# Performance work log

Measured on AMD Instinct MI355X. Metric: run time of the kernel, lower is better.

## Reference

```python
import jax, jax.numpy as jnp
import numpy as np

N, E, IN, H, C, EDIM, G, NC = 20000, 200000, 512, 4, 64, 384, 64, 751
NEG_GATV2 = 0.2   # leaky_relu slope inside GATv2 attention
NEG_ACT = 0.01    # F.leaky_relu default between layers


def _w(key, shape):
    return jax.random.normal(key, shape, dtype=jnp.float32) * 0.05


def setup_inputs() -> dict:
    key = jax.random.key(0)
    ks = jax.random.split(key, 24)
    x = jax.random.normal(ks[0], (N, IN), dtype=jnp.float32)
    edge_index = jax.random.randint(ks[1], (2, E), 0, N, dtype=jnp.int32)
    edge_attr = jax.random.normal(ks[2], (E, EDIM), dtype=jnp.float32)
    batch = (jnp.arange(N, dtype=jnp.int32) * G) // N  # sorted, covers all G graphs
    return {
        "x": x, "edge_index": edge_index, "edge_attr": edge_attr, "batch": batch,
        # GATv2 layer 1 (512 -> 4 heads x 64, concat)
        "W1l": _w(ks[3], (IN, H * C)), "b1l": jnp.zeros((H * C,), jnp.float32),
        "W1r": _w(ks[4], (IN, H * C)), "b1r": jnp.zeros((H * C,), jnp.float32),
        "W1e": _w(ks[5], (EDIM, H * C)),
        "att1": _w(ks[6], (H, C)), "bias1": jnp.zeros((H * C,), jnp.float32),
        # GATv2 layer 2 (256 -> 1 head x 64)
        "W2l": _w(ks[7], (H * C, C)), "b2l": jnp.zeros((C,), jnp.float32),
        "W2r": _w(ks[8], (H * C, C)), "b2r": jnp.zeros((C,), jnp.float32),
        "W2e": _w(ks[9], (EDIM, C)),
        "att2": _w(ks[10], (1, C)), "bias2": jnp.zeros((C,), jnp.float32),
        # LayerNorm + classifier
        "ln_g": jnp.ones((C,), jnp.float32), "ln_b": jnp.zeros((C,), jnp.float32),
        "clf_W": _w(ks[11], (C, NC)), "clf_b": jnp.zeros((NC,), jnp.float32),
    }


def gatv2_layer(x, ei_i, ei_j, ea, Wl, bl, Wr, br, We, att, bias, heads, outc):
    n = x.shape[0]
    xl = (x @ Wl + bl).reshape(n, heads, outc)  # source-side transform (x_j)
    xr = (x @ Wr + br).reshape(n, heads, outc)  # target-side transform (x_i)
    ep = (ea @ We).reshape(-1, heads, outc)     # lin_edge has no bias in PyG
    m = jax.nn.leaky_relu(xl[ei_j] + xr[ei_i] + ep, NEG_GATV2)  # [E',H,C]
    logit = jnp.einsum('ehc,hc->eh', m, att)
    lmax = jax.ops.segment_max(logit, ei_i, num_segments=n)
    ex = jnp.exp(logit - lmax[ei_i])
    den = jax.ops.segment_sum(ex, ei_i, num_segments=n)
    alpha = ex / den[ei_i]                                       # segment softmax
    out = jax.ops.segment_sum(xl[ei_j] * alpha[:, :, None], ei_i, num_segments=n)
    return out.reshape(n, heads * outc) + bias, alpha


def reference(x, edge_index, edge_attr, batch, W1l, b1l, W1r, b1r, W1e, att1, bias1,
              W2l, b2l, W2r, b2r, W2e, att2, bias2, ln_g, ln_b, clf_W, clf_b):
    n = x.shape[0]
    row, col = edge_index[0], edge_index[1]
    # add_self_loops with fill_value='mean': loop attr = scatter-mean over edge_index[1]
    cnt = jax.ops.segment_sum(jnp.ones_like(edge_attr[:, 0]), col, num_segments=n)
    loop_attr = jax.ops.segment_sum(edge_attr, col, num_segments=n) / jnp.maximum(cnt, 1.0)[:, None]
    loops = jnp.arange(n, dtype=row.dtype)
    # flow='target_to_source': aggregate at i=edge_index[0], messages from j=edge_index[1]
    ei_i = jnp.concatenate([row, loops])
    ei_j = jnp.concatenate([col, loops])
    ea = jnp.concatenate([edge_attr, loop_attr], axis=0)

    h1, _ = gatv2_layer(x, ei_i, ei_j, ea, W1l, b1l, W1r, b1r, W1e, att1, bias1, H, C)
    h1 = jax.nn.leaky_relu(h1, NEG_ACT)
    h2, _ = gatv2_layer(h1, ei_i, ei_j, ea, W2l, b2l, W2r, b2r, W2e, att2, bias2, 1, C)
    h2 = jax.nn.leaky_relu(h2, NEG_ACT)

    g = jax.ops.segment_max(h2, batch, num_segments=G)  # global_max_pool -> [G, C]
    mu = g.mean(axis=-1, keepdims=True)
    var = g.var(axis=-1, keepdims=True)
    gn = (g - mu) / jnp.sqrt(var + 1e-5) * ln_g + ln_b
    cls_score = gn @ clf_W + clf_b
    return cls_score, gn
```

## Files before the change

### kernel.cpp

```cpp
#include <hip/hip_runtime.h>

#define NN 20000
#define NE 200000
#define NH1 256
#define ED 384
#define NG 64
#define NCLS 751
#define ETOT (NE + NN)

typedef unsigned short u16;
typedef __attribute__((ext_vector_type(8))) short short8;
typedef __attribute__((ext_vector_type(4))) float f32x4;

__device__ __forceinline__ float bf2f(u16 u){
  union { unsigned int i; float f; } v; v.i = ((unsigned int)u) << 16; return v.f;
}
__device__ __forceinline__ u16 f2bf(float f){
  union { float f; unsigned int i; } v; v.f = f;
  return (u16)((v.i + 0x7fffu + ((v.i >> 16) & 1u)) >> 16);
}

__global__ void transpose_k(const float* __restrict__ in, u16* __restrict__ out, int K, int N){
  int idx = blockIdx.x * 256 + threadIdx.x;
  if (idx >= K * N) return;
  int k = idx / N, n = idx - k * N;
  out[n * K + k] = f2bf(in[idx]);
}

__global__ void convx_k(const float* __restrict__ in, u16* __restrict__ out, int total8){
  int idx = blockIdx.x * 256 + threadIdx.x;
  if (idx >= total8) return;
  const float4* p = (const float4*)in + (size_t)idx * 2;
  float4 f0 = p[0], f1 = p[1];
  union { u16 h[8]; uint4 v; } pk;
  pk.h[0] = f2bf(f0.x); pk.h[1] = f2bf(f0.y); pk.h[2] = f2bf(f0.z); pk.h[3] = f2bf(f0.w);
  pk.h[4] = f2bf(f1.x); pk.h[5] = f2bf(f1.y); pk.h[6] = f2bf(f1.z); pk.h[7] = f2bf(f1.w);
  ((uint4*)out)[idx] = pk.v;
}

__global__ void concatbias_k(const float* __restrict__ b1l, const float* __restrict__ b1r,
                             const float* __restrict__ b2l, const float* __restrict__ b2r,
                             float* __restrict__ biasLR1, float* __restrict__ biasLR2){
  int i = blockIdx.x * 256 + threadIdx.x;
  if (i < 256) biasLR1[i] = b1l[i];
  else if (i < 512) biasLR1[i] = b1r[i - 256];
  else if (i < 576) biasLR2[i - 512] = b2l[i - 512];
  else if (i < 640) biasLR2[i - 512] = b2r[i - 576];
}

__global__ void hist_k(const int* __restrict__ rowA, const int* __restrict__ colA,
                       int* __restrict__ degR, int* __restrict__ degC){
  int e = blockIdx.x * 256 + threadIdx.x;
  if (e >= NE) return;
  atomicAdd(&degR[rowA[e]], 1);
  atomicAdd(&degC[colA[e]], 1);
}

__global__ void scan_k(const int* __restrict__ degR, const int* __restrict__ degC,
                       int* __restrict__ rowPtr, int* __restrict__ colPtr){
  __shared__ int sR[256], sC[256];
  int t = threadIdx.x;
  const int chunk = (NN + 255) / 256;
  int beg = t * chunk, end = min(beg + chunk, NN);
  int aR = 0, aC = 0;
  for (int i = beg; i < end; i++){ aR += degR[i]; aC += degC[i]; }
  sR[t] = aR; sC[t] = aC;
  __syncthreads();
  for (int off = 1; off < 256; off <<= 1){
    int vR = 0, vC = 0;
    if (t >= off){ vR = sR[t - off]; vC = sC[t - off]; }
    __syncthreads();
    sR[t] += vR; sC[t] += vC;
    __syncthreads();
  }
  int rR = (t == 0) ? 0 : sR[t - 1];
  int rC = (t == 0) ? 0 : sC[t - 1];
  for (int i = beg; i < end; i++){
    rowPtr[i] = rR; rR += degR[i];
    colPtr[i] = rC; rC += degC[i];
  }
  if (t == 255){ rowPtr[NN] = sR[255]; colPtr[NN] = sC[255]; }
}

__global__ void scatter_k(const int* __restrict__ rowA, const int* __restrict__ colA,
                          const int* __restrict__ rowPtr, const int* __restrict__ colPtr,
                          int* __restrict__ rowCur, int* __restrict__ colCur,
                          int* __restrict__ rowIdx, int* __restrict__ colIdx){
  int e = blockIdx.x * 256 + threadIdx.x;
  if (e >= NE) return;
  int r = rowA[e]; int p = atomicAdd(&rowCur[r], 1); rowIdx[rowPtr[r] + p] = e;
  int c = colA[e]; int q = atomicAdd(&colCur[c], 1); colIdx[colPtr[c] + q] = e;
}

__global__ __launch_bounds__(256) void loopattr_k(const int* __restrict__ colPtr,
                                                  const int* __restrict__ colIdx,
                                                  const float* __restrict__ eattr,
                                                  u16* __restrict__ ea16){
  int node = blockIdx.x * 4 + (threadIdx.x >> 6);
  if (node >= NN) return;
  int lane = threadIdx.x & 63;
  int p0 = colPtr[node], deg = colPtr[node + 1] - p0;
  float inv = 1.f / fmaxf((float)deg, 1.f);
  float s[6] = {0.f, 0.f, 0.f, 0.f, 0.f, 0.f};
  for (int t = 0; t < deg; t++){
    int e = colIdx[p0 + t];
    const float* rowp = eattr + (size_t)e * ED;
    u16* wp = ea16 + (size_t)e * ED;
    #pragma unroll
    for (int c0 = 0; c0 < 6; c0++){
      float v = rowp[c0 * 64 + lane];
      s[c0] += v;
      wp[c0 * 64 + lane] = f2bf(v);
    }
  }
  u16* outp = ea16 + (size_t)(NE + node) * ED;
  #pragma unroll
  for (int c0 = 0; c0 < 6; c0++) outp[c0 * 64 + lane] = f2bf(s[c0] * inv);
}

__global__ __launch_bounds__(256)
void gemm_k(const u16* __restrict__ A16,
            const u16* __restrict__ Bt, int M, int K, int Ntot,
            const float* __restrict__ bias, u16* __restrict__ outBf)
{
  __shared__ __align__(16) u16 lA[128 * 40];
  __shared__ __align__(16) u16 lB[64 * 40];
  const int tid  = threadIdx.x;
  const int lane = tid & 63;
  const int wave = tid >> 6;
  const int m0 = blockIdx.x * 128;
  const int n0 = blockIdx.y * 64;
  const int lr  = tid >> 2;
  const int lkc = (tid & 3) << 3;
  const int lm = lane & 15;
  const int lk = (lane >> 4) << 3;
  const int wrow = wave << 5;

  f32x4 acc[2][4];
  #pragma unroll
  for (int i = 0; i < 2; i++)
    #pragma unroll
    for (int j = 0; j < 4; j++) acc[i][j] = (f32x4){0.f, 0.f, 0.f, 0.f};

  const u16* aB0 = A16 + (size_t)(m0 + lr) * K + lkc;
  const u16* aB1 = A16 + (size_t)(m0 + lr + 64) * K + lkc;
  const u16* bB  = Bt + (size_t)(n0 + lr) * K + lkc;

  uint4 rA0, rA1, rB;

#define GEMM_ISSUE(K0) \
  { rA0 = *(const uint4*)(aB0 + (K0)); \
    rA1 = *(const uint4*)(aB1 + (K0)); \
    rB  = *(const uint4*)(bB  + (K0)); }

  GEMM_ISSUE(0);
  for (int k0 = 0; k0 < K; k0 += 32){
    *(uint4*)(&lA[lr * 40 + lkc]) = rA0;
    *(uint4*)(&lA[(lr + 64) * 40 + lkc]) = rA1;
    *(uint4*)(&lB[lr * 40 + lkc]) = rB;
    __syncthreads();
    if (k0 + 32 < K) GEMM_ISSUE(k0 + 32);
    short8 a0 = *(const short8*)(&lA[(wrow + lm) * 40 + lk]);
    short8 a1 = *(const short8*)(&lA[(wrow + 16 + lm) * 40 + lk]);
    #pragma unroll
    for (int nj = 0; nj < 4; nj++){
      short8 b = *(const short8*)(&lB[(nj * 16 + lm) * 40 + lk]);
      acc[0][nj] = __builtin_amdgcn_mfma_f32_16x16x32_bf16(a0, b, acc[0][nj], 0, 0, 0);
      acc[1][nj] = __builtin_amdgcn_mfma_f32_16x16x32_bf16(a1, b, acc[1][nj], 0, 0, 0);
    }
    __syncthreads();
  }
#undef GEMM_ISSUE

  #pragma unroll
  for (int mi = 0; mi < 2; mi++)
    #pragma unroll
    for (int r4 = 0; r4 < 4; r4++){
      int row = wrow + mi * 16 + ((lane >> 4) << 2) + r4;
      int gm = m0 + row;
      if (gm < M){
        #pragma unroll
        for (int nj = 0; nj < 4; nj++){
          int gc = n0 + nj * 16 + lm;
          outBf[(size_t)gm * Ntot + gc] = f2bf(acc[mi][nj][r4] + bias[gc]);
        }
      }
    }
}

__global__ __launch_bounds__(256)
void edge_k(const u16* __restrict__ ea16,
            const u16* __restrict__ BtE,
            const int* __restrict__ rowA, const int* __restrict__ colA,
            const u16* __restrict__ XLR1,
            const float* __restrict__ att1,
            float* __restrict__ logit1,
            u16* __restrict__ ep2)
{
  __shared__ __align__(16) u16 lA[64 * 40];
  __shared__ __align__(16) u16 lB[320 * 40];
  const int tid = threadIdx.x;
  const int lane = tid & 63;
  const int wave = tid >> 6;
  const int m0 = blockIdx.x * 64;
  const int lm = lane & 15;
  const int lk = (lane >> 4) << 3;
  const int arow = tid >> 2;
  const int akc = (tid & 3) << 3;

  f32x4 acc[4][5];
  #pragma unroll
  for (int i = 0; i < 4; i++)
    #pragma unroll
    for (int j = 0; j < 5; j++) acc[i][j] = (f32x4){0.f, 0.f, 0.f, 0.f};

  const int gmA = m0 + arow;
  const u16* aBase = ea16 + (size_t)gmA * ED + akc;
  const u16* bBase = BtE + (size_t)arow * ED + akc;

  uint4 pA, pB0, pB1, pB2, pB3, pB4;

#define EDGE_ISSUE(K0) \
  { pA  = *(const uint4*)(aBase + (K0)); \
    const u16* bp = bBase + (K0); \
    pB0 = *(const uint4*)(bp); \
    pB1 = *(const uint4*)(bp + (size_t)64 * ED); \
    pB2 = *(const uint4*)(bp + (size_t)128 * ED); \
    pB3 = *(const uint4*)(bp + (size_t)192 * ED); \
    pB4 = *(const uint4*)(bp + (size_t)256 * ED); }

  EDGE_ISSUE(0);
  for (int k0 = 0; k0 < ED; k0 += 32){
    *(uint4*)(&lA[arow * 40 + akc]) = pA;
    *(uint4*)(&lB[(arow      ) * 40 + akc]) = pB0;
    *(uint4*)(&lB[(arow +  64) * 40 + akc]) = pB1;
    *(uint4*)(&lB[(arow + 128) * 40 + akc]) = pB2;
    *(uint4*)(&lB[(arow + 192) * 40 + akc]) = pB3;
    *(uint4*)(&lB[(arow + 256) * 40 + akc]) = pB4;
    __syncthreads();
    if (k0 + 32 < ED) EDGE_ISSUE(k0 + 32);
    short8 a[4];
    #pragma unroll
    for (int mi = 0; mi < 4; mi++) a[mi] = *(const short8*)(&lA[(mi * 16 + lm) * 40 + lk]);
    #pragma unroll
    for (int nj = 0; nj < 4; nj++){
      short8 b = *(const short8*)(&lB[(wave * 64 + nj * 16 + lm) * 40 + lk]);
      #pragma unroll
      for (int mi = 0; mi < 4; mi++)
        acc[mi][nj] = __builtin_amdgcn_mfma_f32_16x16x32_bf16(a[mi], b, acc[mi][nj], 0, 0, 0);
    }
    {
      short8 b = *(const short8*)(&lB[(256 + wave * 16 + lm) * 40 + lk]);
      #pragma unroll
      for (int mi = 0; mi < 4; mi++)
        acc[mi][4] = __builtin_amdgcn_mfma_f32_16x16x32_bf16(a[mi], b, acc[mi][4], 0, 0, 0);
    }
    __syncthreads();
  }
#undef EDGE_ISSUE

  float attc[4];
  #pragma unroll
  for (int nj = 0; nj < 4; nj++) attc[nj] = att1[wave * 64 + nj * 16 + lm];
  const int quad4 = (lane >> 4) << 2;
  #pragma unroll
  for (int mi = 0; mi < 4; mi++)
    #pragma unroll
    for (int r4 = 0; r4 < 4; r4++){
      int e = m0 + mi * 16 + quad4 + r4;
      float partial = 0.f;
      if (e < ETOT){
        int ii = (e < NE) ? rowA[e] : (e - NE);
        int jj = (e < NE) ? colA[e] : (e - NE);
        const u16* xlp = XLR1 + (size_t)jj * 512 + wave * 64;
        const u16* xrp = XLR1 + (size_t)ii * 512 + 256 + wave * 64;
        #pragma unroll
        for (int nj = 0; nj < 4; nj++){
          float v = acc[mi][nj][r4] + bf2f(xlp[nj * 16 + lm]) + bf2f(xrp[nj * 16 + lm]);
          v = (v > 0.f) ? v : 0.2f * v;
          partial += v * attc[nj];
        }
        ep2[(size_t)e * 64 + wave * 16 + lm] = f2bf(acc[mi][4][r4]);
      }
      partial += __shfl_xor(partial, 1);
      partial += __shfl_xor(partial, 2);
      partial += __shfl_xor(partial, 4);
      partial += __shfl_xor(partial, 8);
      if (lm == 0 && e < ETOT) logit1[(size_t)e * 4 + wave] = partial;
    }
}

__global__ __launch_bounds__(256) void logit2_k(const int* __restrict__ rowA,
    const int* __restrict__ colA, const u16* __restrict__ ep2,
    const u16* __restrict__ XLR2,
    const float* __restrict__ att2, float* __restrict__ logit2)
{
  int e = blockIdx.x * 16 + (threadIdx.x >> 4);
  if (e >= ETOT) return;
  int lm = threadIdx.x & 15;
  int ii = (e < NE) ? rowA[e] : (e - NE);
  int jj = (e < NE) ? colA[e] : (e - NE);
  ushort4 pe = *(const ushort4*)(ep2 + (size_t)e * 64 + lm * 4);
  ushort4 pl = *(const ushort4*)(XLR2 + (size_t)jj * 128 + lm * 4);
  ushort4 pr = *(const ushort4*)(XLR2 + (size_t)ii * 128 + 64 + lm * 4);
  float s = 0.f;
  float v0 = bf2f(pe.x) + bf2f(pl.x) + bf2f(pr.x); v0 = v0 > 0.f ? v0 : 0.2f * v0;
  float v1 = bf2f(pe.y) + bf2f(pl.y) + bf2f(pr.y); v1 = v1 > 0.f ? v1 : 0.2f * v1;
  float v2 = bf2f(pe.z) + bf2f(pl.z) + bf2f(pr.z); v2 = v2 > 0.f ? v2 : 0.2f * v2;
  float v3 = bf2f(pe.w) + bf2f(pl.w) + bf2f(pr.w); v3 = v3 > 0.f ? v3 : 0.2f * v3;
  s = v0 * att2[lm * 4] + v1 * att2[lm * 4 + 1] + v2 * att2[lm * 4 + 2] + v3 * att2[lm * 4 + 3];
  s += __shfl_xor(s, 1);
  s += __shfl_xor(s, 2);
  s += __shfl_xor(s, 4);
  s += __shfl_xor(s, 8);
  if (lm == 0) logit2[e] = s;
}

__global__ __launch_bounds__(256) void agg1_k(const int* __restrict__ rowPtr,
    const int* __restrict__ rowIdx, const float4* __restrict__ lg4,
    const u16* __restrict__ XL1, int xstride, const int* __restrict__ colA,
    const float* __restrict__ bias1, u16* __restrict__ H1)
{
  int node = blockIdx.x * 4 + (threadIdx.x >> 6);
  if (node >= NN) return;
  int lane = threadIdx.x & 63;
  int p0 = rowPtr[node], deg = rowPtr[node + 1] - p0;
  float4 sl = lg4[NE + node];
  float m0 = sl.x, m1 = sl.y, m2 = sl.z, m3 = sl.w;
  for (int t = lane; t < deg; t += 64){
    float4 l = lg4[rowIdx[p0 + t]];
    m0 = fmaxf(m0, l.x); m1 = fmaxf(m1, l.y); m2 = fmaxf(m2, l.z); m3 = fmaxf(m3, l.w);
  }
  #pragma unroll
  for (int off = 32; off > 0; off >>= 1){
    m0 = fmaxf(m0, __shfl_xor(m0, off));
    m1 = fmaxf(m1, __shfl_xor(m1, off));
    m2 = fmaxf(m2, __shfl_xor(m2, off));
    m3 = fmaxf(m3, __shfl_xor(m3, off));
  }
  float d0, d1, d2, d3, a0, a1, a2, a3;
  {
    float e0 = __expf(sl.x - m0), e1 = __expf(sl.y - m1), e2 = __expf(sl.z - m2), e3 = __expf(sl.w - m3);
    d0 = e0; d1 = e1; d2 = e2; d3 = e3;
    const u16* xp = XL1 + (size_t)node * xstride;
    a0 = e0 * bf2f(xp[lane]); a1 = e1 * bf2f(xp[64 + lane]);
    a2 = e2 * bf2f(xp[128 + lane]); a3 = e3 * bf2f(xp[192 + lane]);
  }
  int t = 0;
  for (; t + 1 < deg; t += 2){
    int eA = rowIdx[p0 + t];
    int eB = rowIdx[p0 + t + 1];
    float4 lA_ = lg4[eA];
    float4 lB_ = lg4[eB];
    int jA = colA[eA];
    int jB = colA[eB];
    const u16* xa = XL1 + (size_t)jA * xstride;
    const u16* xb = XL1 + (size_t)jB * xstride;
    float eA0 = __expf(lA_.x - m0), eA1 = __expf(lA_.y - m1), eA2 = __expf(lA_.z - m2), eA3 = __expf(lA_.w - m3);
    float eB0 = __expf(lB_.x - m0), eB1 = __expf(lB_.y - m1), eB2 = __expf(lB_.z - m2), eB3 = __expf(lB_.w - m3);
    d0 += eA0 + eB0; d1 += eA1 + eB1; d2 += eA2 + eB2; d3 += eA3 + eB3;
    a0 += eA0 * bf2f(xa[lane])       + eB0 * bf2f(xb[lane]);
    a1 += eA1 * bf2f(xa[64 + lane])  + eB1 * bf2f(xb[64 + lane]);
    a2 += eA2 * bf2f(xa[128 + lane]) + eB2 * bf2f(xb[128 + lane]);
    a3 += eA3 * bf2f(xa[192 + lane]) + eB3 * bf2f(xb[192 + lane]);
  }
  if (t < deg){
    int e = rowIdx[p0 + t];
    float4 l = lg4[e];
    int j = colA[e];
    float e0 = __expf(l.x - m0), e1 = __expf(l.y - m1), e2 = __expf(l.z - m2), e3 = __expf(l.w - m3);
    d0 += e0; d1 += e1; d2 += e2; d3 += e3;
    const u16* xp = XL1 + (size_t)j * xstride;
    a0 += e0 * bf2f(xp[lane]); a1 += e1 * bf2f(xp[64 + lane]);
    a2 += e2 * bf2f(xp[128 + lane]); a3 += e3 * bf2f(xp[192 + lane]);
  }
  float v0 = a0 / d0 + bias1[lane];
  float v1 = a1 / d1 + bias1[64 + lane];
  float v2 = a2 / d2 + bias1[128 + lane];
  float v3 = a3 / d3 + bias1[192 + lane];
  v0 = v0 > 0.f ? v0 : 0.01f * v0;
  v1 = v1 > 0.f ? v1 : 0.01f * v1;
  v2 = v2 > 0.f ? v2 : 0.01f * v2;
  v3 = v3 > 0.f ? v3 : 0.01f * v3;
  u16* hp = H1 + (size_t)node * NH1;
  hp[lane] = f2bf(v0); hp[64 + lane] = f2bf(v1);
  hp[128 + lane] = f2bf(v2); hp[192 + lane] = f2bf(v3);
}

__global__ __launch_bounds__(256) void agg2_k(const int* __restrict__ rowPtr,
    const int* __restrict__ rowIdx, const float* __restrict__ lg,
    const u16* __restrict__ XL2, int xstride, const int* __restrict__ colA,
    const float* __restrict__ bias2, float* __restrict__ H2)
{
  int node = blockIdx.x * 4 + (threadIdx.x >> 6);
  if (node >= NN) return;
  int lane = threadIdx.x & 63;
  int p0 = rowPtr[node], deg = rowPtr[node + 1] - p0;
  float sl = lg[NE + node];
  float mx = sl;
  for (int t = lane; t < deg; t += 64) mx = fmaxf(mx, lg[rowIdx[p0 + t]]);
  #pragma unroll
  for (int off = 32; off > 0; off >>= 1) mx = fmaxf(mx, __shfl_xor(mx, off));
  float den = __expf(sl - mx);
  float acc = den * bf2f(XL2[(size_t)node * xstride + lane]);
  int t = 0;
  for (; t + 1 < deg; t += 2){
    int eA = rowIdx[p0 + t];
    int eB = rowIdx[p0 + t + 1];
    float exA = __expf(lg[eA] - mx);
    float exB = __expf(lg[eB] - mx);
    int jA = colA[eA];
    int jB = colA[eB];
    den += exA + exB;
    acc += exA * bf2f(XL2[(size_t)jA * xstride + lane])
         + exB * bf2f(XL2[(size_t)jB * xstride + lane]);
  }
  if (t < deg){
    int e = rowIdx[p0 + t];
    float ex = __expf(lg[e] - mx);
    den += ex;
    acc += ex * bf2f(XL2[(size_t)colA[e] * xstride + lane]);
  }
  float v = acc / den + bias2[lane];
  v = v > 0.f ? v : 0.01f * v;
  H2[(size_t)node * 64 + lane] = v;
}

__global__ __launch_bounds__(256) void poolln_k(const float* __restrict__ H2,
    const float* __restrict__ lng, const float* __restrict__ lnb, float* __restrict__ outGn)
{
  __shared__ float sm[4][64];
  int g = blockIdx.x, w = threadIdx.x >> 6, c = threadIdx.x & 63;
  int beg = (g * NN + NG - 1) / NG;
  int end = ((g + 1) * NN + NG - 1) / NG;
  float m = -3.0e38f;
  for (int n = beg + w; n < end; n += 4) m = fmaxf(m, H2[(size_t)n * 64 + c]);
  sm[w][c] = m;
  __syncthreads();
  if (threadIdx.x < 64){
    m = fmaxf(fmaxf(sm[0][c], sm[1][c]), fmaxf(sm[2][c], sm[3][c]));
    float s = m;
    #pragma unroll
    for (int off = 32; off > 0; off >>= 1) s += __shfl_xor(s, off);
    float mu = s * (1.f / 64.f);
    float d = m - mu;
    float vv = d * d;
    #pragma unroll
    for (int off = 32; off > 0; off >>= 1) vv += __shfl_xor(vv, off);
    float var = vv * (1.f / 64.f);
    outGn[g * 64 + c] = d * rsqrtf(var + 1e-5f) * lng[c] + lnb[c];
  }
}

__global__ __launch_bounds__(256) void clf_k(const float* __restrict__ gn,
    const float* __restrict__ W, const float* __restrict__ b, float* __restrict__ outCls)
{
  __shared__ float sg[64];
  int g = blockIdx.x;
  if (threadIdx.x < 64) sg[threadIdx.x] = gn[g * 64 + threadIdx.x];
  __syncthreads();
  for (int o = threadIdx.x; o < NCLS; o += 256){
    float s = b[o];
    #pragma unroll 16
    for (int c = 0; c < 64; c++) s += sg[c] * W[c * NCLS + o];
    outCls[(size_t)g * NCLS + o] = s;
  }
}

extern "C" void kernel_launch(void* const* d_in, const int* in_sizes, int n_in,
                              void* d_out, int out_size, void* d_ws, size_t ws_size,
                              hipStream_t stream)
{
  const float* x     = (const float*)d_in[0];
  const int*   eidx  = (const int*)d_in[1];
  const float* eattr = (const float*)d_in[2];
  const float* W1l = (const float*)d_in[4];
  const float* b1l = (const float*)d_in[5];
  const float* W1r = (const float*)d_in[6];
  const float* b1r = (const float*)d_in[7];
  const float* W1e = (const float*)d_in[8];
  const float* att1 = (const float*)d_in[9];
  const float* bias1 = (const float*)d_in[10];
  const float* W2l = (const float*)d_in[11];
  const float* b2l = (const float*)d_in[12];
  const float* W2r = (const float*)d_in[13];
  const float* b2r = (const float*)d_in[14];
  const float* W2e = (const float*)d_in[15];
  const float* att2 = (const float*)d_in[16];
  const float* bias2 = (const float*)d_in[17];
  const float* lng = (const float*)d_in[18];
  const float* lnb = (const float*)d_in[19];
  const float* clfW = (const float*)d_in[20];
  const float* clfb = (const float*)d_in[21];
  const int* rowA = eidx;
  const int* colA = eidx + NE;

  char* w = (char*)d_ws;
  auto alloc = [&](size_t b) -> char* {
    char* p = w; w += (b + 255) & ~(size_t)255; return p;
  };
  u16* W1lrT  = (u16*)alloc((size_t)512 * 512 * 2);
  u16* BtE    = (u16*)alloc((size_t)320 * ED * 2);
  u16* W2lrT  = (u16*)alloc((size_t)128 * 256 * 2);
  float* biasLR1 = (float*)alloc(512 * 4);
  float* biasLR2 = (float*)alloc(128 * 4);
  int* degR   = (int*)alloc((size_t)NN * 4);
  int* degC   = (int*)alloc((size_t)NN * 4);
  int* rowPtr = (int*)alloc((size_t)(NN + 1) * 4);
  int* colPtr = (int*)alloc((size_t)(NN + 1) * 4);
  int* rowCur = (int*)alloc((size_t)NN * 4);
  int* colCur = (int*)alloc((size_t)NN * 4);
  int* rowIdx = (int*)alloc((size_t)NE * 4);
  int* colIdx = (int*)alloc((size_t)NE * 4);
  u16* ea16   = (u16*)alloc((size_t)ETOT * ED * 2);
  u16* x16    = (u16*)alloc((size_t)NN * 512 * 2);
  u16* XLR1   = (u16*)alloc((size_t)NN * 512 * 2);
  float* logit1 = (float*)alloc((size_t)ETOT * 4 * 4);
  u16* H1     = (u16*)alloc((size_t)NN * NH1 * 2);
  u16* ep2    = (u16*)alloc((size_t)ETOT * 64 * 2);
  u16* XLR2   = (u16*)ea16;
  float* logit2 = (float*)((char*)ea16 + (size_t)5500928);
  float* H2   = (float*)((char*)ea16 + (size_t)6553600);

  hipMemsetAsync(degR, 0, (size_t)NN * 4, stream);
  hipMemsetAsync(degC, 0, (size_t)NN * 4, stream);
  hipMemsetAsync(rowCur, 0, (size_t)NN * 4, stream);
  hipMemsetAsync(colCur, 0, (size_t)NN * 4, stream);

  transpose_k<<<(512 * 256 + 255) / 256, 256, 0, stream>>>(W1l, W1lrT, 512, 256);
  transpose_k<<<(512 * 256 + 255) / 256, 256, 0, stream>>>(W1r, W1lrT + (size_t)256 * 512, 512, 256);
  transpose_k<<<(ED * 256 + 255) / 256, 256, 0, stream>>>(W1e, BtE, ED, 256);
  transpose_k<<<(ED * 64 + 255) / 256, 256, 0, stream>>>(W2e, BtE + (size_t)256 * ED, ED, 64);
  transpose_k<<<(256 * 64 + 255) / 256, 256, 0, stream>>>(W2l, W2lrT, 256, 64);
  transpose_k<<<(256 * 64 + 255) / 256, 256, 0, stream>>>(W2r, W2lrT + (size_t)64 * 256, 256, 64);
  concatbias_k<<<3, 256, 0, stream>>>(b1l, b1r, b2l, b2r, biasLR1, biasLR2);
  convx_k<<<(NN * 512 / 8 + 255) / 256, 256, 0, stream>>>(x, x16, NN * 512 / 8);

  hist_k<<<(NE + 255) / 256, 256, 0, stream>>>(rowA, colA, degR, degC);
  scan_k<<<1, 256, 0, stream>>>(degR, degC, rowPtr, colPtr);
  scatter_k<<<(NE + 255) / 256, 256, 0, stream>>>(rowA, colA, rowPtr, colPtr,
                                                  rowCur, colCur, rowIdx, colIdx);
  loopattr_k<<<(NN + 3) / 4, 256, 0, stream>>>(colPtr, colIdx, eattr, ea16);

  dim3 gx1((NN + 127) / 128, 8);
  gemm_k<<<gx1, 256, 0, stream>>>(x16, W1lrT, NN, 512, 512, biasLR1, XLR1);
  edge_k<<<(ETOT + 63) / 64, 256, 0, stream>>>(ea16, BtE, rowA, colA,
                                               XLR1, att1, logit1, ep2);
  agg1_k<<<(NN + 3) / 4, 256, 0, stream>>>(rowPtr, rowIdx, (const float4*)logit1,
                                           XLR1, 512, colA, bias1, H1);
  dim3 gx2((NN + 127) / 128, 2);
  gemm_k<<<gx2, 256, 0, stream>>>(H1, W2lrT, NN, 256, 128, biasLR2, XLR2);
  logit2_k<<<(ETOT + 15) / 16, 256, 0, stream>>>(rowA, colA, ep2, XLR2, att2, logit2);
  agg2_k<<<(NN + 3) / 4, 256, 0, stream>>>(rowPtr, rowIdx, logit2, XLR2, 128, colA, bias2, H2);

  float* outCls = (float*)d_out;
  float* outGn  = outCls + (size_t)NG * NCLS;
  poolln_k<<<NG, 256, 0, stream>>>(H2, lng, lnb, outGn);
  clf_k<<<NG, 256, 0, stream>>>(outGn, clfW, clfb, outCls);
}
```

Measured before the change: 962.7 us.

## Widen GEMM N-tile to 128 and deepen A prefetch in GEMM and edge kernels

The node GEMM now computes 128x128 tiles per block instead of 128x64, halving grid columns and reusing each A tile across twice as many MFMAs. Both the node GEMM and the edge GEMM unroll the K loop by two and prefetch A fragments two steps ahead to hide global latency. The edge kernel also gets an occupancy hint of four blocks per CU. Trade-offs are higher register pressure from doubled accumulators, fewer blocks for the smaller second GEMM, and prefetches that read slightly past the last K slice.

```diff
diff --git a/kernel.cpp b/kernel.cpp
--- a/kernel.cpp
+++ b/kernel.cpp
@@ -124,53 +124,74 @@
             const float* __restrict__ bias, u16* __restrict__ outBf)
 {
   __shared__ __align__(16) u16 lA[128 * 40];
-  __shared__ __align__(16) u16 lB[64 * 40];
+  __shared__ __align__(16) u16 lB[128 * 40];
   const int tid  = threadIdx.x;
   const int lane = tid & 63;
   const int wave = tid >> 6;
   const int m0 = blockIdx.x * 128;
-  const int n0 = blockIdx.y * 64;
+  const int n0 = blockIdx.y * 128;
   const int lr  = tid >> 2;
   const int lkc = (tid & 3) << 3;
   const int lm = lane & 15;
   const int lk = (lane >> 4) << 3;
   const int wrow = wave << 5;
 
-  f32x4 acc[2][4];
+  f32x4 acc[2][8];
   #pragma unroll
   for (int i = 0; i < 2; i++)
     #pragma unroll
-    for (int j = 0; j < 4; j++) acc[i][j] = (f32x4){0.f, 0.f, 0.f, 0.f};
+    for (int j = 0; j < 8; j++) acc[i][j] = (f32x4){0.f, 0.f, 0.f, 0.f};
 
   const u16* aB0 = A16 + (size_t)(m0 + lr) * K + lkc;
   const u16* aB1 = A16 + (size_t)(m0 + lr + 64) * K + lkc;
-  const u16* bB  = Bt + (size_t)(n0 + lr) * K + lkc;
-
-  uint4 rA0, rA1, rB;
-
-#define GEMM_ISSUE(K0) \
-  { rA0 = *(const uint4*)(aB0 + (K0)); \
-    rA1 = *(const uint4*)(aB1 + (K0)); \
-    rB  = *(const uint4*)(bB  + (K0)); }
-
-  GEMM_ISSUE(0);
-  for (int k0 = 0; k0 < K; k0 += 32){
-    *(uint4*)(&lA[lr * 40 + lkc]) = rA0;
-    *(uint4*)(&lA[(lr + 64) * 40 + lkc]) = rA1;
-    *(uint4*)(&lB[lr * 40 + lkc]) = rB;
-    __syncthreads();
-    if (k0 + 32 < K) GEMM_ISSUE(k0 + 32);
-    short8 a0 = *(const short8*)(&lA[(wrow + lm) * 40 + lk]);
-    short8 a1 = *(const short8*)(&lA[(wrow + 16 + lm) * 40 + lk]);
-    #pragma unroll
-    for (int nj = 0; nj < 4; nj++){
-      short8 b = *(const short8*)(&lB[(nj * 16 + lm) * 40 + lk]);
-      acc[0][nj] = __builtin_amdgcn_mfma_f32_16x16x32_bf16(a0, b, acc[0][nj], 0, 0, 0);
-      acc[1][nj] = __builtin_amdgcn_mfma_f32_16x16x32_bf16(a1, b, acc[1][nj], 0, 0, 0);
-    }
-    __syncthreads();
-  }
-#undef GEMM_ISSUE
+  const u16* bB0 = Bt + (size_t)(n0 + lr) * K + lkc;
+  const u16* bB1 = Bt + (size_t)(n0 + lr + 64) * K + lkc;
+
+  uint4 rAa0, rAa1, rAb0, rAb1, rB0, rB1;
+
+#define GSTORE(RA0, RA1) \
+  { *(uint4*)(&lA[lr * 40 + lkc]) = RA0; \
+    *(uint4*)(&lA[(lr + 64) * 40 + lkc]) = RA1; \
+    *(uint4*)(&lB[lr * 40 + lkc]) = rB0; \
+    *(uint4*)(&lB[(lr + 64) * 40 + lkc]) = rB1; }
+
+#define GCOMP \
+  { short8 a0 = *(const short8*)(&lA[(wrow + lm) * 40 + lk]); \
+    short8 a1 = *(const short8*)(&lA[(wrow + 16 + lm) * 40 + lk]); \
+    _Pragma("unroll") \
+    for (int nj = 0; nj < 8; nj++){ \
+      short8 b = *(const short8*)(&lB[(nj * 16 + lm) * 40 + lk]); \
+      acc[0][nj] = __builtin_amdgcn_mfma_f32_16x16x32_bf16(a0, b, acc[0][nj], 0, 0, 0); \
+      acc[1][nj] = __builtin_amdgcn_mfma_f32_16x16x32_bf16(a1, b, acc[1][nj], 0, 0, 0); \
+    } }
+
+  rAa0 = *(const uint4*)(aB0);
+  rAa1 = *(const uint4*)(aB1);
+  rAb0 = *(const uint4*)(aB0 + 32);
+  rAb1 = *(const uint4*)(aB1 + 32);
+  rB0  = *(const uint4*)(bB0);
+  rB1  = *(const uint4*)(bB1);
+
+  for (int k0 = 0; k0 < K; k0 += 64){
+    GSTORE(rAa0, rAa1);
+    __syncthreads();
+    rAa0 = *(const uint4*)(aB0 + k0 + 64);
+    rAa1 = *(const uint4*)(aB1 + k0 + 64);
+    rB0  = *(const uint4*)(bB0 + k0 + 32);
+    rB1  = *(const uint4*)(bB1 + k0 + 32);
+    GCOMP;
+    __syncthreads();
+    GSTORE(rAb0, rAb1);
+    __syncthreads();
+    rAb0 = *(const uint4*)(aB0 + k0 + 96);
+    rAb1 = *(const uint4*)(aB1 + k0 + 96);
+    rB0  = *(const uint4*)(bB0 + k0 + 64);
+    rB1  = *(const uint4*)(bB1 + k0 + 64);
+    GCOMP;
+    __syncthreads();
+  }
+#undef GSTORE
+#undef GCOMP
 
   #pragma unroll
   for (int mi = 0; mi < 2; mi++)
@@ -180,7 +201,7 @@
       int gm = m0 + row;
       if (gm < M){
         #pragma unroll
-        for (int nj = 0; nj < 4; nj++){
+        for (int nj = 0; nj < 8; nj++){
           int gc = n0 + nj * 16 + lm;
           outBf[(size_t)gm * Ntot + gc] = f2bf(acc[mi][nj][r4] + bias[gc]);
         }
@@ -188,7 +209,7 @@
     }
 }
 
-__global__ __launch_bounds__(256)
+__global__ __launch_bounds__(256, 4)
 void edge_k(const u16* __restrict__ ea16,
             const u16* __restrict__ BtE,
             const int* __restrict__ rowA, const int* __restrict__ colA,
@@ -218,46 +239,61 @@
   const u16* aBase = ea16 + (size_t)gmA * ED + akc;
   const u16* bBase = BtE + (size_t)arow * ED + akc;
 
-  uint4 pA, pB0, pB1, pB2, pB3, pB4;
-
-#define EDGE_ISSUE(K0) \
-  { pA  = *(const uint4*)(aBase + (K0)); \
-    const u16* bp = bBase + (K0); \
+  uint4 pAa, pAb, pB0, pB1, pB2, pB3, pB4;
+
+#define EISS_B(K0) \
+  { const u16* bp = bBase + (K0); \
     pB0 = *(const uint4*)(bp); \
     pB1 = *(const uint4*)(bp + (size_t)64 * ED); \
     pB2 = *(const uint4*)(bp + (size_t)128 * ED); \
     pB3 = *(const uint4*)(bp + (size_t)192 * ED); \
     pB4 = *(const uint4*)(bp + (size_t)256 * ED); }
 
-  EDGE_ISSUE(0);
-  for (int k0 = 0; k0 < ED; k0 += 32){
-    *(uint4*)(&lA[arow * 40 + akc]) = pA;
-    *(uint4*)(&lB[(arow      ) * 40 + akc]) = pB0;
-    *(uint4*)(&lB[(arow +  64) * 40 + akc]) = pB1;
-    *(uint4*)(&lB[(arow + 128) * 40 + akc]) = pB2;
-    *(uint4*)(&lB[(arow + 192) * 40 + akc]) = pB3;
-    *(uint4*)(&lB[(arow + 256) * 40 + akc]) = pB4;
-    __syncthreads();
-    if (k0 + 32 < ED) EDGE_ISSUE(k0 + 32);
-    short8 a[4];
-    #pragma unroll
-    for (int mi = 0; mi < 4; mi++) a[mi] = *(const short8*)(&lA[(mi * 16 + lm) * 40 + lk]);
-    #pragma unroll
-    for (int nj = 0; nj < 4; nj++){
-      short8 b = *(const short8*)(&lB[(wave * 64 + nj * 16 + lm) * 40 + lk]);
-      #pragma unroll
-      for (int mi = 0; mi < 4; mi++)
-        acc[mi][nj] = __builtin_amdgcn_mfma_f32_16x16x32_bf16(a[mi], b, acc[mi][nj], 0, 0, 0);
-    }
-    {
-      short8 b = *(const short8*)(&lB[(256 + wave * 16 + lm) * 40 + lk]);
-      #pragma unroll
-      for (int mi = 0; mi < 4; mi++)
-        acc[mi][4] = __builtin_amdgcn_mfma_f32_16x16x32_bf16(a[mi], b, acc[mi][4], 0, 0, 0);
-    }
-    __syncthreads();
-  }
-#undef EDGE_ISSUE
+#define ESTORE(PA) \
+  { *(uint4*)(&lA[arow * 40 + akc]) = PA; \
+    *(uint4*)(&lB[(arow      ) * 40 + akc]) = pB0; \
+    *(uint4*)(&lB[(arow +  64) * 40 + akc]) = pB1; \
+    *(uint4*)(&lB[(arow + 128) * 40 + akc]) = pB2; \
+    *(uint4*)(&lB[(arow + 192) * 40 + akc]) = pB3; \
+    *(uint4*)(&lB[(arow + 256) * 40 + akc]) = pB4; }
+
+#define ECOMP \
+  { short8 a[4]; \
+    _Pragma("unroll") \
+    for (int mi = 0; mi < 4; mi++) a[mi] = *(const short8*)(&lA[(mi * 16 + lm) * 40 + lk]); \
+    _Pragma("unroll") \
+    for (int nj = 0; nj < 4; nj++){ \
+      short8 b = *(const short8*)(&lB[(wave * 64 + nj * 16 + lm) * 40 + lk]); \
+      _Pragma("unroll") \
+      for (int mi = 0; mi < 4; mi++) \
+        acc[mi][nj] = __builtin_amdgcn_mfma_f32_16x16x32_bf16(a[mi], b, acc[mi][nj], 0, 0, 0); \
+    } \
+    { short8 b = *(const short8*)(&lB[(256 + wave * 16 + lm) * 40 + lk]); \
+      _Pragma("unroll") \
+      for (int mi = 0; mi < 4; mi++) \
+        acc[mi][4] = __builtin_amdgcn_mfma_f32_16x16x32_bf16(a[mi], b, acc[mi][4], 0, 0, 0); } }
+
+  pAa = *(const uint4*)(aBase);
+  pAb = *(const uint4*)(aBase + 32);
+  EISS_B(0);
+
+  for (int k0 = 0; k0 < ED; k0 += 64){
+    ESTORE(pAa);
+    __syncthreads();
+    pAa = *(const uint4*)(aBase + k0 + 64);
+    EISS_B(k0 + 32);
+    ECOMP;
+    __syncthreads();
+    ESTORE(pAb);
+    __syncthreads();
+    pAb = *(const uint4*)(aBase + k0 + 96);
+    EISS_B(k0 + 64);
+    ECOMP;
+    __syncthreads();
+  }
+#undef EISS_B
+#undef ESTORE
+#undef ECOMP
 
   float attc[4];
   #pragma unroll
@@ -542,13 +578,13 @@
                                                   rowCur, colCur, rowIdx, colIdx);
   loopattr_k<<<(NN + 3) / 4, 256, 0, stream>>>(colPtr, colIdx, eattr, ea16);
 
-  dim3 gx1((NN + 127) / 128, 8);
+  dim3 gx1((NN + 127) / 128, 4);
   gemm_k<<<gx1, 256, 0, stream>>>(x16, W1lrT, NN, 512, 512, biasLR1, XLR1);
   edge_k<<<(ETOT + 63) / 64, 256, 0, stream>>>(ea16, BtE, rowA, colA,
                                                XLR1, att1, logit1, ep2);
   agg1_k<<<(NN + 3) / 4, 256, 0, stream>>>(rowPtr, rowIdx, (const float4*)logit1,
                                            XLR1, 512, colA, bias1, H1);
-  dim3 gx2((NN + 127) / 128, 2);
+  dim3 gx2((NN + 127) / 128, 1);
   gemm_k<<<gx2, 256, 0, stream>>>(H1, W2lrT, NN, 256, 128, biasLR2, XLR2);
   logit2_k<<<(ETOT + 15) / 16, 256, 0, stream>>>(rowA, colA, ep2, XLR2, att2, logit2);
   agg2_k<<<(NN + 3) / 4, 256, 0, stream>>>(rowPtr, rowIdx, logit2, XLR2, 128, colA, bias2, H2);
```

Measured after the change: 983.3 us. 2.1% more time.
